# Kernel optimization log

Measured on AMD Instinct MI355X. Metric: run time of the kernel, lower is better.

The kernel has to match this reference:

```python
import jax, jax.numpy as jnp
import numpy as np

B, N, D, H = 4, 2048, 256, 8
d = D // H          # 32 per-head dim
EPS = 1e-5
SCALE = 1.0 / float(np.sqrt(d))


def setup_inputs() -> dict:
    key = jax.random.key(0)
    ks = jax.random.split(key, 6)
    s = 0.02
    x = jax.random.normal(ks[0], (B, N, D), jnp.float32)
    # RoPE frequencies: theta_j = 10000^(-2j/d), angle = pos * theta
    inv_freq = 1.0 / (10000.0 ** (jnp.arange(0, d, 2, dtype=jnp.float32) / d))  # (d/2,)
    ang = jnp.arange(N, dtype=jnp.float32)[:, None] * inv_freq[None, :]          # (N, d/2)
    return {
        "x": x,
        "freqs_cos": jnp.cos(ang),
        "freqs_sin": jnp.sin(ang),
        "w_qkv": jax.random.normal(ks[1], (D, 3 * D), jnp.float32) * s,
        "b_qkv": jnp.zeros((3 * D,), jnp.float32),
        "w_proj": jax.random.normal(ks[2], (D, D), jnp.float32) * s,
        "b_proj": jnp.zeros((D,), jnp.float32),
        "ln1_g": jnp.ones((D,), jnp.float32),
        "ln1_b": jnp.zeros((D,), jnp.float32),
        "ln2_g": jnp.ones((D,), jnp.float32),
        "ln2_b": jnp.zeros((D,), jnp.float32),
        "w1": jax.random.normal(ks[3], (D, 2 * D), jnp.float32) * s,
        "b1": jnp.zeros((2 * D,), jnp.float32),
        "w2": jax.random.normal(ks[4], (2 * D, D), jnp.float32) * s,
        "b2": jnp.zeros((D,), jnp.float32),
    }


def _layer_norm(x, g, b):
    mu = jnp.mean(x, axis=-1, keepdims=True)
    var = jnp.mean(jnp.square(x - mu), axis=-1, keepdims=True)
    return (x - mu) * jax.lax.rsqrt(var + EPS) * g + b


def _rope(t, cos, sin):
    # t: (B,H,N,d); interleaved (even,odd) pairs viewed as complex, multiplied by e^{i*ang}
    tr = t.reshape(B, H, N, d // 2, 2)
    te, to = tr[..., 0], tr[..., 1]
    c = cos[None, None, :, :]
    s = sin[None, None, :, :]
    oe = te * c - to * s
    oo = te * s + to * c
    return jnp.stack([oe, oo], axis=-1).reshape(B, H, N, d)


def reference(x, freqs_cos, freqs_sin, w_qkv, b_qkv, w_proj, b_proj,
              ln1_g, ln1_b, ln2_g, ln2_b, w1, b1, w2, b2):
    # Pre-LN MHSA with RoPE (dropout = identity at eval)
    h = _layer_norm(x, ln1_g, ln1_b)
    qkv = (h @ w_qkv + b_qkv).reshape(B, N, 3, H, d).transpose(0, 2, 3, 1, 4)  # (B,3,H,N,d)
    q, k, v = qkv[:, 0], qkv[:, 1], qkv[:, 2]
    q = _rope(q, freqs_cos, freqs_sin)
    k = _rope(k, freqs_cos, freqs_sin)
    attn = jax.nn.softmax(jnp.einsum('bhnd,bhmd->bhnm', q, k) * SCALE, axis=-1)
    out = jnp.einsum('bhnm,bhmd->bhnd', attn, v).transpose(0, 2, 1, 3).reshape(B, N, D)
    x = x + (out @ w_proj + b_proj)
    h = _layer_norm(x, ln2_g, ln2_b)
    ffn = jax.nn.relu(h @ w1 + b1) @ w2 + b2
    return x + ffn
```

## Files before the change

kernel.cpp:

```cpp
#include <hip/hip_runtime.h>
#include <hip/hip_bf16.h>
#include <math.h>

#define Bsz 4
#define Nseq 2048
#define Dm 256
#define Hh 8
#define Hd 32
#define EPS_ 1e-5f
#define SCALE_ 0.17677669529663687f
#define QSC_ (0.17677669529663687f * 1.4426950408889634f)

typedef __attribute__((ext_vector_type(8))) short short8;
typedef __attribute__((ext_vector_type(4))) short short4v;
typedef __attribute__((ext_vector_type(4))) float f32x4;
typedef __attribute__((ext_vector_type(16))) float f32x16;

__device__ __forceinline__ void gload16(const void* g, void* l) {
    __builtin_amdgcn_global_load_lds(
        (const __attribute__((address_space(1))) void*)g,
        (__attribute__((address_space(3))) void*)l, 16, 0, 0);
}

__device__ __forceinline__ short bf16s(float f) {
    __hip_bfloat16 h = __float2bfloat16(f);
    return *(short*)&h;
}

union FU { float f; unsigned u; };

__device__ __forceinline__ int pk2bf(float a, float b) {
    FU ua, ub; ua.f = a; ub.f = b;
    return (int)__builtin_amdgcn_perm(ub.u, ua.u, 0x07060302u);
}

union I4S8 { int i[4]; short8 s; };

__global__ __launch_bounds__(256) void prep_kernel(
    const float* __restrict__ x, const float* __restrict__ g1,
    const float* __restrict__ b1v, __hip_bfloat16* __restrict__ hout,
    const float* __restrict__ s0, const float* __restrict__ s1,
    const float* __restrict__ s2, const float* __restrict__ s3,
    __hip_bfloat16* __restrict__ d0, __hip_bfloat16* __restrict__ d1,
    __hip_bfloat16* __restrict__ d2, __hip_bfloat16* __restrict__ d3) {
    __shared__ float t[32][33];
    if (blockIdx.x < 2048) {
        int row  = blockIdx.x * 4 + (threadIdx.x >> 6);
        int lane = threadIdx.x & 63;
        const float* xr = x + (size_t)row * Dm;
        float4 v = *(const float4*)(xr + lane * 4);
        float s  = v.x + v.y + v.z + v.w;
        float ss = v.x * v.x + v.y * v.y + v.z * v.z + v.w * v.w;
        #pragma unroll
        for (int off = 32; off; off >>= 1) {
            s  += __shfl_xor(s, off);
            ss += __shfl_xor(ss, off);
        }
        float mu  = s * (1.0f / Dm);
        float var = ss * (1.0f / Dm) - mu * mu;
        float rs  = rsqrtf(var + EPS_);
        float4 gv = *(const float4*)(g1 + lane * 4);
        float4 bv = *(const float4*)(b1v + lane * 4);
        short4v o4 = { bf16s((v.x - mu) * rs * gv.x + bv.x),
                       bf16s((v.y - mu) * rs * gv.y + bv.y),
                       bf16s((v.z - mu) * rs * gv.z + bv.z),
                       bf16s((v.w - mu) * rs * gv.w + bv.w) };
        *(short4v*)(hout + (size_t)row * Dm + lane * 4) = o4;
        return;
    }
    int bid = blockIdx.x - 2048;
    const float* src; __hip_bfloat16* dst; int K, N, tb;
    if (bid < 192)      { src = s0; dst = d0; K = 256; N = 768; tb = bid; }
    else if (bid < 256) { src = s1; dst = d1; K = 256; N = 256; tb = bid - 192; }
    else if (bid < 384) { src = s2; dst = d2; K = 256; N = 512; tb = bid - 256; }
    else                { src = s3; dst = d3; K = 512; N = 256; tb = bid - 384; }
    int tn = N >> 5;
    int k0 = (tb / tn) * 32, n0 = (tb % tn) * 32;
    int c = threadIdx.x & 31, r0 = threadIdx.x >> 5;
    #pragma unroll
    for (int i = 0; i < 4; i++) {
        int r = r0 + i * 8;
        t[r][c] = src[(size_t)(k0 + r) * N + n0 + c];
    }
    __syncthreads();
    #pragma unroll
    for (int i = 0; i < 4; i++) {
        int n = r0 + i * 8;
        dst[(size_t)(n0 + n) * K + k0 + c] = __float2bfloat16(t[c][n]);
    }
}

__global__ __launch_bounds__(256) void qkv_mfma(const __hip_bfloat16* __restrict__ A,
                                                const __hip_bfloat16* __restrict__ Wt,
                                                const float* __restrict__ bias,
                                                const float* __restrict__ fcos,
                                                const float* __restrict__ fsin,
                                                __hip_bfloat16* __restrict__ qout,
                                                __hip_bfloat16* __restrict__ kout,
                                                __hip_bfloat16* __restrict__ vt) {
    const int K = 256;
    __shared__ __align__(16) __hip_bfloat16 As[2][64 * 64];
    __shared__ __align__(16) __hip_bfloat16 Bs[2][64 * 64];
    const int tid = threadIdx.x, w = tid >> 6, lane = tid & 63;
    const int lm = lane & 15, lq = lane >> 4;
    const int bm = blockIdx.y * 64, bn = blockIdx.x * 64;
    f32x4 acc[4];
    #pragma unroll
    for (int j = 0; j < 4; j++) acc[j] = (f32x4){0.f, 0.f, 0.f, 0.f};

    const int sr = tid >> 3, ssl = tid & 7;
    const int sgk = (ssl ^ (sr & 7)) * 8;
    const int sr2 = 32 + sr;
    const int sgk2 = (ssl ^ (sr2 & 7)) * 8;

    gload16(A + (size_t)(bm + sr) * K + sgk, &As[0][w * 512]);
    gload16(A + (size_t)(bm + sr2) * K + sgk2, &As[0][2048 + w * 512]);
    gload16(Wt + (size_t)(bn + sr) * K + sgk, &Bs[0][w * 512]);
    gload16(Wt + (size_t)(bn + sr2) * K + sgk2, &Bs[0][2048 + w * 512]);

    const int arow = w * 16 + lm;
    const int ar7 = arow & 7;
    for (int t = 0; t < K / 64; t++) {
        const int buf = t & 1;
        __syncthreads();
        if (t + 1 < K / 64) {
            int k0 = (t + 1) * 64;
            gload16(A + (size_t)(bm + sr) * K + k0 + sgk, &As[buf ^ 1][w * 512]);
            gload16(A + (size_t)(bm + sr2) * K + k0 + sgk2, &As[buf ^ 1][2048 + w * 512]);
            gload16(Wt + (size_t)(bn + sr) * K + k0 + sgk, &Bs[buf ^ 1][w * 512]);
            gload16(Wt + (size_t)(bn + sr2) * K + k0 + sgk2, &Bs[buf ^ 1][2048 + w * 512]);
        }
        #pragma unroll
        for (int ks = 0; ks < 2; ks++) {
            short8 a = *(const short8*)&As[buf][arow * 64 + (((ks * 4 + lq) ^ ar7) * 8)];
            #pragma unroll
            for (int nf = 0; nf < 4; nf++) {
                int cc = nf * 16 + lm;
                short8 bfr = *(const short8*)&Bs[buf][cc * 64 + (((ks * 4 + lq) ^ (cc & 7)) * 8)];
                acc[nf] = __builtin_amdgcn_mfma_f32_16x16x32_bf16(a, bfr, acc[nf], 0, 0, 0);
            }
        }
    }
    const int seg = bn >> 8;
    #pragma unroll
    for (int nf = 0; nf < 4; nf++) {
        int cg = bn + nf * 16 + lm;
        int hh = (cg & 255) >> 5;
        int dd = (nf & 1) * 16 + lm;
        int i0 = dd >> 1;
        float bi = bias[cg];
        #pragma unroll
        for (int r = 0; r < 4; r++) {
            int rg = bm + w * 16 + lq * 4 + r;
            int bb = rg >> 11, n = rg & (Nseq - 1);
            float v = acc[nf][r] + bi;
            if (seg == 2) {
                vt[(((size_t)(bb * Hh + hh)) * Hd + dd) * Nseq + n] = __float2bfloat16(v);
            } else {
                float vp = __shfl_xor(v, 1);
                float cs = fcos[n * 16 + i0], sn = fsin[n * 16 + i0];
                float outv = (dd & 1) ? (vp * sn + v * cs) : (v * cs - vp * sn);
                if (seg == 0) outv *= QSC_;
                __hip_bfloat16* dst = (seg == 0) ? qout : kout;
                dst[(((size_t)(bb * Hh + hh)) * Nseq + n) * Hd + dd] = __float2bfloat16(outv);
            }
        }
    }
}

__global__ __launch_bounds__(256) void attn_mfma(const __hip_bfloat16* __restrict__ q,
                                                 const __hip_bfloat16* __restrict__ k,
                                                 const __hip_bfloat16* __restrict__ vt,
                                                 __hip_bfloat16* __restrict__ att) {
    __shared__ __align__(16) char smem[4096 + 16384 + 16384 + 512];
    __hip_bfloat16* Qs  = (__hip_bfloat16*)smem;
    __hip_bfloat16* KsB = (__hip_bfloat16*)(smem + 4096);
    __hip_bfloat16* VsB = (__hip_bfloat16*)(smem + 20480);
    float* RedO = (float*)(smem + 4096);
    float* RedS = (float*)(smem + 4096 + 8192);
    float* smS  = (float*)(smem + 4096 + 8192 + 256);

    const int tid = threadIdx.x, w = tid >> 6, lane = tid & 63;
    const int l31 = lane & 31, hi = lane >> 5;
    const int wq = w >> 1, wk = w & 1;
    const int bh = blockIdx.y, qbase = blockIdx.x * 64;
    const __hip_bfloat16* qp = q + ((size_t)bh * Nseq + qbase) * Hd;
    const __hip_bfloat16* kp = k + (size_t)bh * Nseq * Hd;
    const __hip_bfloat16* vp = vt + (size_t)bh * Hd * Nseq;
    const int r8 = tid >> 3, s8 = tid & 7;

    {
        int r = tid >> 2, sl = tid & 3;
        gload16(qp + r * 32 + ((sl ^ (r & 3)) * 8), Qs + w * 512);
    }
    #pragma unroll
    for (int par = 0; par < 2; par++) {
        gload16(kp + (par * 64 + 2 * r8 + (s8 >> 2)) * 32 + (((s8 & 3) ^ (r8 & 3)) * 8),
                KsB + par * 2048 + w * 512);
        gload16(vp + (size_t)r8 * Nseq + par * 64 + ((s8 ^ (r8 & 7)) * 8),
                VsB + par * 2048 + w * 512);
    }
    __syncthreads();

    const int qrow = wq * 32 + l31;
    short8 qf0 = *(const short8*)&Qs[qrow * 32 + ((hi ^ (l31 & 3)) * 8)];
    short8 qf1 = *(const short8*)&Qs[qrow * 32 + (((2 + hi) ^ (l31 & 3)) * 8)];

    f32x16 O;
    #pragma unroll
    for (int i = 0; i < 16; i++) O[i] = 0.f;
    float sm = 0.f;

    for (int t = 0; t < 16; t++) {
        const int buf = t & 1;
        if (t + 1 < 16) {
            const int kb2 = (t + 1) * 128;
            #pragma unroll
            for (int par = 0; par < 2; par++) {
                gload16(kp + (kb2 + par * 64 + 2 * r8 + (s8 >> 2)) * 32 + (((s8 & 3) ^ (r8 & 3)) * 8),
                        KsB + ((buf ^ 1) * 2 + par) * 2048 + w * 512);
                gload16(vp + (size_t)r8 * Nseq + kb2 + par * 64 + ((s8 ^ (r8 & 7)) * 8),
                        VsB + ((buf ^ 1) * 2 + par) * 2048 + w * 512);
            }
        }
        const __hip_bfloat16* Kc = KsB + (buf * 2 + wk) * 2048;
        const __hip_bfloat16* Vc = VsB + (buf * 2 + wk) * 2048;
        f32x16 St0, St1;
        #pragma unroll
        for (int i = 0; i < 16; i++) { St0[i] = 0.f; St1[i] = 0.f; }
        {
            int pr = l31 >> 1, elb = pr * 64 + (l31 & 1) * 32;
            short8 kf0 = *(const short8*)&Kc[elb + ((hi ^ (pr & 3)) * 8)];
            short8 kf1 = *(const short8*)&Kc[elb + (((2 + hi) ^ (pr & 3)) * 8)];
            St0 = __builtin_amdgcn_mfma_f32_32x32x16_bf16(kf0, qf0, St0, 0, 0, 0);
            St0 = __builtin_amdgcn_mfma_f32_32x32x16_bf16(kf1, qf1, St0, 0, 0, 0);
        }
        {
            int pr = 16 + (l31 >> 1), elb = pr * 64 + (l31 & 1) * 32;
            short8 kf0 = *(const short8*)&Kc[elb + ((hi ^ (pr & 3)) * 8)];
            short8 kf1 = *(const short8*)&Kc[elb + (((2 + hi) ^ (pr & 3)) * 8)];
            St1 = __builtin_amdgcn_mfma_f32_32x32x16_bf16(kf0, qf0, St1, 0, 0, 0);
            St1 = __builtin_amdgcn_mfma_f32_32x32x16_bf16(kf1, qf1, St1, 0, 0, 0);
        }
        int pk0[8], pk1[8];
        #pragma unroll
        for (int p = 0; p < 8; p++) {
            float a = __builtin_amdgcn_exp2f(St0[2 * p]);
            float b = __builtin_amdgcn_exp2f(St0[2 * p + 1]);
            sm += a + b;
            pk0[p] = pk2bf(a, b);
        }
        #pragma unroll
        for (int p = 0; p < 8; p++) {
            float a = __builtin_amdgcn_exp2f(St1[2 * p]);
            float b = __builtin_amdgcn_exp2f(St1[2 * p + 1]);
            sm += a + b;
            pk1[p] = pk2bf(a, b);
        }
        #pragma unroll
        for (int tt = 0; tt < 4; tt++) {
            const int* PK = (tt >> 1) ? pk1 : pk0;
            const int base = 4 * (tt & 1);
            int keep0 = hi ? PK[base + 2] : PK[base + 0];
            int keep1 = hi ? PK[base + 3] : PK[base + 1];
            int send0 = hi ? PK[base + 0] : PK[base + 2];
            int send1 = hi ? PK[base + 1] : PK[base + 3];
            int x0 = __shfl_xor(send0, 32);
            int x1 = __shfl_xor(send1, 32);
            I4S8 u;
            u.i[0] = hi ? x0 : keep0;
            u.i[1] = hi ? x1 : keep1;
            u.i[2] = hi ? keep0 : x0;
            u.i[3] = hi ? keep1 : x1;
            short8 vf = *(const short8*)&Vc[l31 * 64 + (((2 * tt + hi) ^ (l31 & 7)) * 8)];
            O = __builtin_amdgcn_mfma_f32_32x32x16_bf16(u.s, vf, O, 0, 0, 0);
        }
        __syncthreads();
    }
    sm += __shfl_xor(sm, 32);
    if (wk == 1) {
        #pragma unroll
        for (int j = 0; j < 16; j++) RedO[(wq * 16 + j) * 64 + lane] = O[j];
        if (hi == 0) RedS[wq * 32 + l31] = sm;
    }
    __syncthreads();
    if (wk == 0) {
        #pragma unroll
        for (int j = 0; j < 16; j++) O[j] += RedO[(wq * 16 + j) * 64 + lane];
        sm += RedS[wq * 32 + l31];
        if (hi == 0) smS[wq * 32 + l31] = sm;
    }
    __syncthreads();
    if (wk == 0) {
        const int bb = bh >> 3, hh = bh & 7;
        #pragma unroll
        for (int m = 0; m < 4; m++) {
            float4 sv = *(const float4*)&smS[wq * 32 + 8 * m + 4 * hi];
            #pragma unroll
            for (int i = 0; i < 4; i++) {
                int n = qbase + wq * 32 + 8 * m + 4 * hi + i;
                att[((size_t)(bb * Nseq + n)) * Dm + hh * Hd + l31] =
                    __float2bfloat16(O[4 * m + i] * (1.0f / sv[i]));
            }
        }
    }
}

__global__ __launch_bounds__(256, 1) void tail_fused(
    const __hip_bfloat16* __restrict__ att, const __hip_bfloat16* __restrict__ wpT,
    const float* __restrict__ b_proj, const float* __restrict__ x,
    const float* __restrict__ g2, const float* __restrict__ bv2,
    const __hip_bfloat16* __restrict__ w1T, const float* __restrict__ b1,
    const __hip_bfloat16* __restrict__ w2T, const float* __restrict__ b2,
    float* __restrict__ out) {
    __shared__ __align__(16) __hip_bfloat16 WS[2][4][4096];
    __shared__ __align__(16) __hip_bfloat16 AH[8192];
    __shared__ __align__(16) __hip_bfloat16 PS[16384];
    __shared__ float red[4][32][2];
    __shared__ float muS[32], rsS[32];

    const int tid = threadIdx.x, w = tid >> 6, lane = tid & 63;
    const int lm = lane & 15, lq = lane >> 4;
    const int R0 = blockIdx.x * 32;
    const int c0 = w * 64;
    const int c0f = w * 128;

    {
        const int srow = tid >> 3, ssl = tid & 7;
        #pragma unroll
        for (int kt = 0; kt < 4; kt++)
            gload16(att + (size_t)(R0 + srow) * 256 + kt * 64 + ((ssl ^ (srow & 7)) * 8),
                    AH + kt * 2048 + w * 512);
    }
    #pragma unroll
    for (int ri = 0; ri < 8; ri++) {
        int r = ri * 8 + (lane >> 3), sl = lane & 7;
        gload16(wpT + (size_t)(c0 + r) * 256 + ((sl ^ (r & 7)) * 8), &WS[0][w][ri * 512]);
    }
    __syncthreads();

    short8 aF[2][4][2];
    #pragma unroll
    for (int mf = 0; mf < 2; mf++) {
        int r = mf * 16 + lm;
        #pragma unroll
        for (int kt = 0; kt < 4; kt++)
            #pragma unroll
            for (int ks = 0; ks < 2; ks++)
                aF[mf][kt][ks] = *(const short8*)&AH[kt * 2048 + r * 64 +
                                                    (((ks * 4 + lq) ^ (lm & 7)) * 8)];
    }
    float xr[2][4][4];
    #pragma unroll
    for (int mf = 0; mf < 2; mf++)
        #pragma unroll
        for (int r = 0; r < 4; r++) {
            int row = R0 + mf * 16 + lq * 4 + r;
            #pragma unroll
            for (int nf = 0; nf < 4; nf++)
                xr[mf][nf][r] = x[(size_t)row * 256 + c0 + nf * 16 + lm];
        }

    f32x4 acc[2][4];
    #pragma unroll
    for (int i = 0; i < 2; i++)
        #pragma unroll
        for (int j = 0; j < 4; j++) acc[i][j] = (f32x4){0.f, 0.f, 0.f, 0.f};
    for (int kt = 0; kt < 4; kt++) {
        const int buf = kt & 1;
        if (kt) __syncthreads();
        if (kt + 1 < 4) {
            #pragma unroll
            for (int ri = 0; ri < 8; ri++) {
                int r = ri * 8 + (lane >> 3), sl = lane & 7;
                gload16(wpT + (size_t)(c0 + r) * 256 + (kt + 1) * 64 + ((sl ^ (r & 7)) * 8),
                        &WS[buf ^ 1][w][ri * 512]);
            }
        }
        #pragma unroll
        for (int ks = 0; ks < 2; ks++)
            #pragma unroll
            for (int nf = 0; nf < 4; nf++) {
                int cc = nf * 16 + lm;
                short8 bfr = *(const short8*)&WS[buf][w][cc * 64 + (((ks * 4 + lq) ^ (lm & 7)) * 8)];
                #pragma unroll
                for (int mf = 0; mf < 2; mf++)
                    acc[mf][nf] = __builtin_amdgcn_mfma_f32_16x16x32_bf16(
                        aF[mf][kt][ks], bfr, acc[mf][nf], 0, 0, 0);
            }
    }
    #pragma unroll
    for (int nf = 0; nf < 4; nf++) {
        float bp = b_proj[c0 + nf * 16 + lm];
        #pragma unroll
        for (int mf = 0; mf < 2; mf++)
            #pragma unroll
            for (int r = 0; r < 4; r++) xr[mf][nf][r] += acc[mf][nf][r] + bp;
    }

    #pragma unroll
    for (int mf = 0; mf < 2; mf++)
        #pragma unroll
        for (int r = 0; r < 4; r++) {
            float s = 0.f, ss = 0.f;
            #pragma unroll
            for (int nf = 0; nf < 4; nf++) {
                float v = xr[mf][nf][r];
                s += v; ss += v * v;
            }
            #pragma unroll
            for (int off = 1; off <= 8; off <<= 1) {
                s  += __shfl_xor(s, off);
                ss += __shfl_xor(ss, off);
            }
            if (lm == 0) {
                int row = mf * 16 + lq * 4 + r;
                red[w][row][0] = s;
                red[w][row][1] = ss;
            }
        }
    #pragma unroll
    for (int ri = 0; ri < 8; ri++) {
        int r = ri * 16 + (lane >> 2), sl = lane & 3;
        gload16(w1T + (size_t)(c0f + r) * 256 + ((sl ^ (r & 3)) * 8), &WS[0][w][ri * 512]);
    }
    __syncthreads();
    if (tid < 32) {
        float s = red[0][tid][0] + red[1][tid][0] + red[2][tid][0] + red[3][tid][0];
        float ss = red[0][tid][1] + red[1][tid][1] + red[2][tid][1] + red[3][tid][1];
        float mu = s * (1.0f / 256.0f);
        muS[tid] = mu;
        rsS[tid] = rsqrtf(ss * (1.0f / 256.0f) - mu * mu + EPS_);
    }
    __syncthreads();
    #pragma unroll
    for (int mf = 0; mf < 2; mf++)
        #pragma unroll
        for (int r = 0; r < 4; r++) {
            int row = mf * 16 + lq * 4 + r;
            float mu = muS[row], rs = rsS[row];
            int rw7 = row & 7;
            #pragma unroll
            for (int nf = 0; nf < 4; nf++) {
                int c = c0 + nf * 16 + lm;
                float h = (xr[mf][nf][r] - mu) * rs * g2[c] + bv2[c];
                int slc = nf * 2 + (lm >> 3);
                AH[w * 2048 + row * 64 + ((slc ^ rw7) * 8) + (lm & 7)] = __float2bfloat16(h);
            }
        }
    __syncthreads();

    f32x4 acc2[2][8];
    #pragma unroll
    for (int i = 0; i < 2; i++)
        #pragma unroll
        for (int j = 0; j < 8; j++) acc2[i][j] = (f32x4){0.f, 0.f, 0.f, 0.f};
    for (int kt = 0; kt < 8; kt++) {
        const int buf = kt & 1;
        if (kt) __syncthreads();
        if (kt + 1 < 8) {
            #pragma unroll
            for (int ri = 0; ri < 8; ri++) {
                int r = ri * 16 + (lane >> 2), sl = lane & 3;
                gload16(w1T + (size_t)(c0f + r) * 256 + (kt + 1) * 32 + ((sl ^ (r & 3)) * 8),
                        &WS[buf ^ 1][w][ri * 512]);
            }
        }
        short8 aA[2];
        #pragma unroll
        for (int mf = 0; mf < 2; mf++) {
            int r = mf * 16 + lm;
            aA[mf] = *(const short8*)&AH[(kt >> 1) * 2048 + r * 64 +
                                         ((((kt & 1) * 4 + lq) ^ (lm & 7)) * 8)];
        }
        #pragma unroll
        for (int nf = 0; nf < 8; nf++) {
            int cc = nf * 16 + lm;
            short8 bfr = *(const short8*)&WS[buf][w][cc * 32 + ((lq ^ (lm & 3)) * 8)];
            #pragma unroll
            for (int mf = 0; mf < 2; mf++)
                acc2[mf][nf] = __builtin_amdgcn_mfma_f32_16x16x32_bf16(
                    aA[mf], bfr, acc2[mf][nf], 0, 0, 0);
        }
    }
    #pragma unroll
    for (int ri = 0; ri < 8; ri++) {
        int r = ri * 8 + (lane >> 3), sl = lane & 7;
        gload16(w2T + (size_t)(c0 + r) * 512 + ((sl ^ (r & 7)) * 8), &WS[0][w][ri * 512]);
    }
    #pragma unroll
    for (int nf = 0; nf < 8; nf++) {
        int c = c0f + nf * 16 + lm;
        float bb1 = b1[c];
        int kt8 = w * 2 + (nf >> 2);
        int slc = (nf & 3) * 2 + (lm >> 3);
        #pragma unroll
        for (int mf = 0; mf < 2; mf++)
            #pragma unroll
            for (int r = 0; r < 4; r++) {
                int row = mf * 16 + lq * 4 + r;
                float p = fmaxf(acc2[mf][nf][r] + bb1, 0.f);
                PS[kt8 * 2048 + row * 64 + ((slc ^ (row & 7)) * 8) + (lm & 7)] =
                    __float2bfloat16(p);
            }
    }
    __syncthreads();

    f32x4 acc3[2][4];
    #pragma unroll
    for (int i = 0; i < 2; i++)
        #pragma unroll
        for (int j = 0; j < 4; j++) acc3[i][j] = (f32x4){0.f, 0.f, 0.f, 0.f};
    for (int kt = 0; kt < 8; kt++) {
        const int buf = kt & 1;
        if (kt) __syncthreads();
        if (kt + 1 < 8) {
            #pragma unroll
            for (int ri = 0; ri < 8; ri++) {
                int r = ri * 8 + (lane >> 3), sl = lane & 7;
                gload16(w2T + (size_t)(c0 + r) * 512 + (kt + 1) * 64 + ((sl ^ (r & 7)) * 8),
                        &WS[buf ^ 1][w][ri * 512]);
            }
        }
        #pragma unroll
        for (int ks = 0; ks < 2; ks++) {
            short8 aP[2];
            #pragma unroll
            for (int mf = 0; mf < 2; mf++) {
                int r = mf * 16 + lm;
                aP[mf] = *(const short8*)&PS[kt * 2048 + r * 64 +
                                             (((ks * 4 + lq) ^ (lm & 7)) * 8)];
            }
            #pragma unroll
            for (int nf = 0; nf < 4; nf++) {
                int cc = nf * 16 + lm;
                short8 bfr = *(const short8*)&WS[buf][w][cc * 64 + (((ks * 4 + lq) ^ (lm & 7)) * 8)];
                #pragma unroll
                for (int mf = 0; mf < 2; mf++)
                    acc3[mf][nf] = __builtin_amdgcn_mfma_f32_16x16x32_bf16(
                        aP[mf], bfr, acc3[mf][nf], 0, 0, 0);
            }
        }
    }
    #pragma unroll
    for (int nf = 0; nf < 4; nf++) {
        int c = c0 + nf * 16 + lm;
        float bb2 = b2[c];
        #pragma unroll
        for (int mf = 0; mf < 2; mf++)
            #pragma unroll
            for (int r = 0; r < 4; r++) {
                int row = R0 + mf * 16 + lq * 4 + r;
                out[(size_t)row * 256 + c] = acc3[mf][nf][r] + bb2 + xr[mf][nf][r];
            }
    }
}

extern "C" void kernel_launch(void* const* d_in, const int* in_sizes, int n_in,
                              void* d_out, int out_size, void* d_ws, size_t ws_size,
                              hipStream_t stream) {
    const float* x      = (const float*)d_in[0];
    const float* fcos   = (const float*)d_in[1];
    const float* fsin   = (const float*)d_in[2];
    const float* w_qkv  = (const float*)d_in[3];
    const float* b_qkv  = (const float*)d_in[4];
    const float* w_proj = (const float*)d_in[5];
    const float* b_proj = (const float*)d_in[6];
    const float* ln1_g  = (const float*)d_in[7];
    const float* ln1_b  = (const float*)d_in[8];
    const float* ln2_g  = (const float*)d_in[9];
    const float* ln2_b  = (const float*)d_in[10];
    const float* w1     = (const float*)d_in[11];
    const float* b1     = (const float*)d_in[12];
    const float* w2     = (const float*)d_in[13];
    const float* b2     = (const float*)d_in[14];
    float* out = (float*)d_out;
    char* base = (char*)d_ws;
    const size_t MB = (size_t)1 << 20;

    __hip_bfloat16* h   = (__hip_bfloat16*)(base);
    __hip_bfloat16* qb  = (__hip_bfloat16*)(base + 4 * MB);
    __hip_bfloat16* kbf = (__hip_bfloat16*)(base + 8 * MB);
    __hip_bfloat16* vtb = (__hip_bfloat16*)(base + 12 * MB);
    __hip_bfloat16* att = (__hip_bfloat16*)(base + 16 * MB);
    __hip_bfloat16* wqT = (__hip_bfloat16*)(base + 20 * MB);
    __hip_bfloat16* wpT = (__hip_bfloat16*)(base + 20 * MB + 393216);
    __hip_bfloat16* w1T = (__hip_bfloat16*)(base + 20 * MB + 524288);
    __hip_bfloat16* w2T = (__hip_bfloat16*)(base + 20 * MB + 786432);

    prep_kernel<<<2560, 256, 0, stream>>>(x, ln1_g, ln1_b, h,
                                          w_qkv, w_proj, w1, w2, wqT, wpT, w1T, w2T);
    qkv_mfma<<<dim3(12, 128), 256, 0, stream>>>(h, wqT, b_qkv, fcos, fsin, qb, kbf, vtb);
    attn_mfma<<<dim3(Nseq / 64, Bsz * Hh), 256, 0, stream>>>(qb, kbf, vtb, att);
    tail_fused<<<256, 256, 0, stream>>>(att, wpT, b_proj, x, ln2_g, ln2_b,
                                        w1T, b1, w2T, b2, out);
}
```

Before: 172.5 us.

## Load K fragments directly to registers and give each wave a private V buffer

The attention kernel no longer stages K through shared memory. Each wave loads its K MFMA fragments straight from global memory into registers and prefetches the next tile's fragments. V is double-buffered in a per-wave LDS region, and manual waitcnt instructions replace the per-iteration block-wide __syncthreads, so waves run independently. This removes block barriers and LDS traffic for K, at the cost of uncoalesced-ish global K reads, more registers, and reliance on the hand-written vmcnt counts being correct.

```diff
diff --git a/kernel.cpp b/kernel.cpp
--- a/kernel.cpp
+++ b/kernel.cpp
@@ -172,10 +172,9 @@
                                                  const __hip_bfloat16* __restrict__ k,
                                                  const __hip_bfloat16* __restrict__ vt,
                                                  __hip_bfloat16* __restrict__ att) {
-    __shared__ __align__(16) char smem[4096 + 16384 + 16384 + 512];
-    __hip_bfloat16* Qs  = (__hip_bfloat16*)smem;
-    __hip_bfloat16* KsB = (__hip_bfloat16*)(smem + 4096);
-    __hip_bfloat16* VsB = (__hip_bfloat16*)(smem + 20480);
+    __shared__ __align__(16) char smem[4096 + 32768 + 512];
+    __hip_bfloat16* Qs = (__hip_bfloat16*)smem;
+    __hip_bfloat16* Vw = (__hip_bfloat16*)(smem + 4096);
     float* RedO = (float*)(smem + 4096);
     float* RedS = (float*)(smem + 4096 + 8192);
     float* smS  = (float*)(smem + 4096 + 8192 + 256);
@@ -187,19 +186,22 @@
     const __hip_bfloat16* qp = q + ((size_t)bh * Nseq + qbase) * Hd;
     const __hip_bfloat16* kp = k + (size_t)bh * Nseq * Hd;
     const __hip_bfloat16* vp = vt + (size_t)bh * Hd * Nseq;
-    const int r8 = tid >> 3, s8 = tid & 7;
 
     {
         int r = tid >> 2, sl = tid & 3;
         gload16(qp + r * 32 + ((sl ^ (r & 3)) * 8), Qs + w * 512);
     }
-    #pragma unroll
-    for (int par = 0; par < 2; par++) {
-        gload16(kp + (par * 64 + 2 * r8 + (s8 >> 2)) * 32 + (((s8 & 3) ^ (r8 & 3)) * 8),
-                KsB + par * 2048 + w * 512);
-        gload16(vp + (size_t)r8 * Nseq + par * 64 + ((s8 ^ (r8 & 7)) * 8),
-                VsB + par * 2048 + w * 512);
-    }
+    __hip_bfloat16* myV = Vw + w * 4096;
+    const int vd = (lane >> 3) & 7, vs = lane & 7;
+    const int szv = (vs ^ vd) * 8;
+    #pragma unroll
+    for (int i = 0; i < 4; i++)
+        gload16(vp + (size_t)(i * 8 + vd) * Nseq + wk * 64 + szv, myV + i * 512);
+    const __hip_bfloat16* kb = kp + (size_t)wk * 64 * Hd + l31 * Hd + hi * 8;
+    short8 kf0 = *(const short8*)(kb);
+    short8 kf1 = *(const short8*)(kb + 16);
+    short8 kf2 = *(const short8*)(kb + 1024);
+    short8 kf3 = *(const short8*)(kb + 1040);
     __syncthreads();
 
     const int qrow = wq * 32 + l31;
@@ -212,36 +214,28 @@
     float sm = 0.f;
 
     for (int t = 0; t < 16; t++) {
-        const int buf = t & 1;
+        const int cur = t & 1;
+        short8 nk0, nk1, nk2, nk3;
         if (t + 1 < 16) {
-            const int kb2 = (t + 1) * 128;
-            #pragma unroll
-            for (int par = 0; par < 2; par++) {
-                gload16(kp + (kb2 + par * 64 + 2 * r8 + (s8 >> 2)) * 32 + (((s8 & 3) ^ (r8 & 3)) * 8),
-                        KsB + ((buf ^ 1) * 2 + par) * 2048 + w * 512);
-                gload16(vp + (size_t)r8 * Nseq + kb2 + par * 64 + ((s8 ^ (r8 & 7)) * 8),
-                        VsB + ((buf ^ 1) * 2 + par) * 2048 + w * 512);
-            }
-        }
-        const __hip_bfloat16* Kc = KsB + (buf * 2 + wk) * 2048;
-        const __hip_bfloat16* Vc = VsB + (buf * 2 + wk) * 2048;
+            const int c = 2 * (t + 1) + wk;
+            asm volatile("s_waitcnt lgkmcnt(0)" ::: "memory");
+            #pragma unroll
+            for (int i = 0; i < 4; i++)
+                gload16(vp + (size_t)(i * 8 + vd) * Nseq + c * 64 + szv,
+                        myV + (cur ^ 1) * 2048 + i * 512);
+            const __hip_bfloat16* kbn = kp + (size_t)c * 64 * Hd + l31 * Hd + hi * 8;
+            nk0 = *(const short8*)(kbn);
+            nk1 = *(const short8*)(kbn + 16);
+            nk2 = *(const short8*)(kbn + 1024);
+            nk3 = *(const short8*)(kbn + 1040);
+        }
         f32x16 St0, St1;
         #pragma unroll
         for (int i = 0; i < 16; i++) { St0[i] = 0.f; St1[i] = 0.f; }
-        {
-            int pr = l31 >> 1, elb = pr * 64 + (l31 & 1) * 32;
-            short8 kf0 = *(const short8*)&Kc[elb + ((hi ^ (pr & 3)) * 8)];
-            short8 kf1 = *(const short8*)&Kc[elb + (((2 + hi) ^ (pr & 3)) * 8)];
-            St0 = __builtin_amdgcn_mfma_f32_32x32x16_bf16(kf0, qf0, St0, 0, 0, 0);
-            St0 = __builtin_amdgcn_mfma_f32_32x32x16_bf16(kf1, qf1, St0, 0, 0, 0);
-        }
-        {
-            int pr = 16 + (l31 >> 1), elb = pr * 64 + (l31 & 1) * 32;
-            short8 kf0 = *(const short8*)&Kc[elb + ((hi ^ (pr & 3)) * 8)];
-            short8 kf1 = *(const short8*)&Kc[elb + (((2 + hi) ^ (pr & 3)) * 8)];
-            St1 = __builtin_amdgcn_mfma_f32_32x32x16_bf16(kf0, qf0, St1, 0, 0, 0);
-            St1 = __builtin_amdgcn_mfma_f32_32x32x16_bf16(kf1, qf1, St1, 0, 0, 0);
-        }
+        St0 = __builtin_amdgcn_mfma_f32_32x32x16_bf16(kf0, qf0, St0, 0, 0, 0);
+        St0 = __builtin_amdgcn_mfma_f32_32x32x16_bf16(kf1, qf1, St0, 0, 0, 0);
+        St1 = __builtin_amdgcn_mfma_f32_32x32x16_bf16(kf2, qf0, St1, 0, 0, 0);
+        St1 = __builtin_amdgcn_mfma_f32_32x32x16_bf16(kf3, qf1, St1, 0, 0, 0);
         int pk0[8], pk1[8];
         #pragma unroll
         for (int p = 0; p < 8; p++) {
@@ -257,6 +251,7 @@
             sm += a + b;
             pk1[p] = pk2bf(a, b);
         }
+        asm volatile("s_waitcnt vmcnt(8)" ::: "memory");
         #pragma unroll
         for (int tt = 0; tt < 4; tt++) {
             const int* PK = (tt >> 1) ? pk1 : pk0;
@@ -272,12 +267,14 @@
             u.i[1] = hi ? x1 : keep1;
             u.i[2] = hi ? keep0 : x0;
             u.i[3] = hi ? keep1 : x1;
-            short8 vf = *(const short8*)&Vc[l31 * 64 + (((2 * tt + hi) ^ (l31 & 7)) * 8)];
+            short8 vf = *(const short8*)&myV[cur * 2048 + l31 * 64 +
+                                            (((2 * tt + hi) ^ (l31 & 7)) * 8)];
             O = __builtin_amdgcn_mfma_f32_32x32x16_bf16(u.s, vf, O, 0, 0, 0);
         }
-        __syncthreads();
+        if (t + 1 < 16) { kf0 = nk0; kf1 = nk1; kf2 = nk2; kf3 = nk3; }
     }
     sm += __shfl_xor(sm, 32);
+    __syncthreads();
     if (wk == 1) {
         #pragma unroll
         for (int j = 0; j < 16; j++) RedO[(wq * 16 + j) * 64 + lane] = O[j];
```

Result: no change. 169.4 us (-1.8%).
